# Optimization experiments

Measured on AMD Instinct MI355X. Metric: run time of the kernel, lower is better.

## Reference

```python
import jax, jax.numpy as jnp
import numpy as np


def _ring_mask(n, d, dtype):
    # concentric-square mask: ring index r = min(i, j, n-1-i, n-1-j);
    # outer d rings are 0, inner rings are 1; center forced to 1.
    i = jnp.arange(n)
    ri = jnp.minimum(i, n - 1 - i)  # [n]
    ring = jnp.minimum(ri[:, None], ri[None, :])  # [n, n]
    mask = (ring >= d).astype(dtype)
    w = (n + 1) // 2
    mask = mask.at[w - 1, w - 1].set(jnp.asarray(1, dtype))
    return mask


def _conv2d(x, w, b):
    # x: [B,1,2,C], w: [1,1,2,k] -> [B,1,1,C] (padding only along last axis)
    pad = (w.shape[3] - 1) // 2
    y = jax.lax.conv_general_dilated(
        x, w, window_strides=(1, 1), padding=((0, 0), (pad, pad)),
        dimension_numbers=('NCHW', 'OIHW', 'NCHW'))
    return y + b.reshape(1, 1, 1, 1)


def setup_inputs() -> dict:
    key = jax.random.key(0)
    k1, k2, k3, k4, k5 = jax.random.split(key, 5)
    B, C1, C2, P = 512, 16, 30, 15
    K = 5  # int((log2(480)+3)/2) made odd
    x = jax.random.normal(k1, (B, C1, C2, P, P), dtype=jnp.float32)
    w1 = jax.random.normal(k2, (1, 1, 2, K), dtype=jnp.float32) * 0.3
    b1 = jax.random.normal(k3, (1,), dtype=jnp.float32) * 0.1
    w2 = jax.random.normal(k4, (1, 1, 2, K), dtype=jnp.float32) * 0.3
    b2 = jax.random.normal(k5, (1,), dtype=jnp.float32) * 0.1
    return {"x": x, "w1": w1, "b1": b1, "w2": w2, "b2": b2}


def reference(x, w1, b1, w2, b2):
    B, C1, C2, H, W = x.shape
    C = C1 * C2
    out = x.reshape(B, C, H, W)
    d = (W - 1) // 2 - 1  # patch_size == W, ScaleMaskModule d
    mask = _ring_mask(W, d, x.dtype)  # [W, W]

    # masked branch: adaptive avg pool(1) == spatial mean of masked input
    out_x1 = (out * mask).mean(axis=(2, 3))  # [B, C]
    out_x2 = out_x1[:, ::-1]                 # reversed channel order
    out_xx = jnp.stack([out_x1, out_x2], axis=1)[:, None]  # [B,1,2,C]

    # plain branch
    out1 = out.mean(axis=(2, 3))  # [B, C]
    out2 = out1[:, ::-1]
    outx = jnp.stack([out1, out2], axis=1)[:, None]  # [B,1,2,C]

    a1 = jax.nn.sigmoid(_conv2d(outx, w1, b1))    # [B,1,1,C]
    a2 = jax.nn.sigmoid(_conv2d(out_xx, w2, b2))  # [B,1,1,C]
    at1 = jnp.transpose(a1 * a2, (0, 3, 1, 2))    # [B,C,1,1]
    at = jax.nn.sigmoid((at1 - 0.2) * 2)

    out = out * at
    return out.reshape(B, C1, C2, H, W)
```

## Files before the change

### kernel.cpp

```cpp
#include <hip/hip_runtime.h>
#include <math.h>

#define BB 512
#define CC 480
#define HW 225
#define CHW (CC * HW)
#define NF4 (CHW / 4)
#define NGRP (CC / 4)
#define NTHREADS 1024
#define NWAVES (NTHREADS / 64)

using f4 = __attribute__((ext_vector_type(4))) float;

__device__ __forceinline__ float sigmoidf(float v) {
    return 1.0f / (1.0f + __expf(-v));
}

__global__ __launch_bounds__(NTHREADS) void fused_kernel(
    const float* __restrict__ x,
    const float* __restrict__ w1, const float* __restrict__ b1,
    const float* __restrict__ w2, const float* __restrict__ b2,
    float* __restrict__ out)
{
    __shared__ float Ms[CC];
    __shared__ float Rs[CC];
    __shared__ float As[CC];

    const int b = blockIdx.x;
    const int t = threadIdx.x;
    const int wave = t >> 6;
    const int lane = t & 63;

    const f4* __restrict__ xb4 = (const f4*)(x + (long long)b * CHW);

    for (int gr = wave; gr < NGRP; gr += NWAVES) {
        const f4* gp = xb4 + gr * 225;
        float f0 = 0.f, f1 = 0.f, f2 = 0.f, f3 = 0.f;
        float r0 = 0.f, r1 = 0.f, r2 = 0.f, r3 = 0.f;
#pragma unroll
        for (int j = 0; j < 4; ++j) {
            const int idx = lane + 64 * j;
            if (idx < 225) {
                f4 v = gp[idx];
                const int e0 = 4 * idx;
#pragma unroll
                for (int jj = 0; jj < 4; ++jj) {
                    const int e = e0 + jj;
                    const float vv = v[jj];
                    const int q = (e >= 450) ? ((e >= 675) ? 3 : 2)
                                             : ((e >= 225) ? 1 : 0);
                    const int r = e - 225 * q;
                    const bool ring = (r >= 96 && r <= 98) ||
                                      (r >= 111 && r <= 113) ||
                                      (r >= 126 && r <= 128);
                    const float rv = ring ? vv : 0.f;
                    f0 += (q == 0) ? vv : 0.f;
                    f1 += (q == 1) ? vv : 0.f;
                    f2 += (q == 2) ? vv : 0.f;
                    f3 += (q == 3) ? vv : 0.f;
                    r0 += (q == 0) ? rv : 0.f;
                    r1 += (q == 1) ? rv : 0.f;
                    r2 += (q == 2) ? rv : 0.f;
                    r3 += (q == 3) ? rv : 0.f;
                }
            }
        }
#pragma unroll
        for (int off = 32; off > 0; off >>= 1) {
            f0 += __shfl_down(f0, off, 64);
            f1 += __shfl_down(f1, off, 64);
            f2 += __shfl_down(f2, off, 64);
            f3 += __shfl_down(f3, off, 64);
            r0 += __shfl_down(r0, off, 64);
            r1 += __shfl_down(r1, off, 64);
            r2 += __shfl_down(r2, off, 64);
            r3 += __shfl_down(r3, off, 64);
        }
        if (lane == 0) {
            const float s = 1.0f / 225.0f;
            Ms[4 * gr + 0] = f0 * s;  Rs[4 * gr + 0] = r0 * s;
            Ms[4 * gr + 1] = f1 * s;  Rs[4 * gr + 1] = r1 * s;
            Ms[4 * gr + 2] = f2 * s;  Rs[4 * gr + 2] = r2 * s;
            Ms[4 * gr + 3] = f3 * s;  Rs[4 * gr + 3] = r3 * s;
        }
    }
    __syncthreads();

    if (t < CC) {
        const int c = t;
        float g1 = b1[0], g2 = b2[0];
#pragma unroll
        for (int k = 0; k < 5; ++k) {
            const int j = c + k - 2;
            if (j >= 0 && j < CC) {
                g1 += w1[k] * Ms[j] + w1[5 + k] * Ms[CC - 1 - j];
                g2 += w2[k] * Rs[j] + w2[5 + k] * Rs[CC - 1 - j];
            }
        }
        As[c] = sigmoidf((sigmoidf(g1) * sigmoidf(g2) - 0.2f) * 2.0f);
    }
    __syncthreads();

    f4* __restrict__ ob4 = (f4*)(out + (long long)b * CHW);
    for (int g = t; g < NF4; g += NTHREADS) {
        f4 v = xb4[g];
        const int e0 = 4 * g;
        const int c0 = e0 / 225;
        const int rr = e0 - 225 * c0;
        const int c1 = c0 + (rr >= 224);
        const int c2 = c0 + (rr >= 223);
        const int c3 = c0 + (rr >= 222);
        v[0] *= As[c0];
        v[1] *= As[c1];
        v[2] *= As[c2];
        v[3] *= As[c3];
        __builtin_nontemporal_store(v, &ob4[g]);
    }
}

extern "C" void kernel_launch(void* const* d_in, const int* in_sizes, int n_in,
                              void* d_out, int out_size, void* d_ws, size_t ws_size,
                              hipStream_t stream)
{
    const float* x  = (const float*)d_in[0];
    const float* w1 = (const float*)d_in[1];
    const float* b1 = (const float*)d_in[2];
    const float* w2 = (const float*)d_in[3];
    const float* b2 = (const float*)d_in[4];
    float* out = (float*)d_out;

    fused_kernel<<<BB, NTHREADS, 0, stream>>>(x, w1, b1, w2, b2, out);
}
```

Baseline: 401.4 us.

## Split fused kernel into reduce, gate, and scale kernels for higher parallelism

Replaces the single per-batch fused kernel with three launches: a grid-stride reduction over all channel groups writing means to workspace, a small gate kernel computing the attention weights, and a chunked scale kernel using 8 blocks per batch. This is meant to raise occupancy and remove the in-block serialization between the reduction and scaling phases. It adds workspace traffic and two extra launches, and it drops any cache reuse of x between the two phases that a single block could have had.

After: 415.9 us. 3.6% more time.

```diff
diff --git a/kernel.cpp b/kernel.cpp
--- a/kernel.cpp
+++ b/kernel.cpp
@@ -7,8 +7,18 @@
 #define CHW (CC * HW)
 #define NF4 (CHW / 4)
 #define NGRP (CC / 4)
-#define NTHREADS 1024
-#define NWAVES (NTHREADS / 64)
+#define NGRP_TOTAL (BB * NGRP)
+
+#define RED_BLOCKS 1920
+#define RED_THREADS 256
+#define RED_WAVES (RED_BLOCKS * (RED_THREADS / 64))
+
+#define CHUNKS 8
+#define CHUNK_F4 (NF4 / CHUNKS)
+#define CHUNK_CH (CC / CHUNKS)
+#define SC_THREADS 256
+#define SC_FULL_ITERS (CHUNK_F4 / SC_THREADS)
+#define SC_TAIL (CHUNK_F4 - SC_FULL_ITERS * SC_THREADS)
 
 using f4 = __attribute__((ext_vector_type(4))) float;
 
@@ -16,25 +26,19 @@
     return 1.0f / (1.0f + __expf(-v));
 }
 
-__global__ __launch_bounds__(NTHREADS) void fused_kernel(
+__global__ __launch_bounds__(RED_THREADS) void reduce_kernel(
     const float* __restrict__ x,
-    const float* __restrict__ w1, const float* __restrict__ b1,
-    const float* __restrict__ w2, const float* __restrict__ b2,
-    float* __restrict__ out)
+    float* __restrict__ S, float* __restrict__ R)
 {
-    __shared__ float Ms[CC];
-    __shared__ float Rs[CC];
-    __shared__ float As[CC];
+    const int wave = threadIdx.x >> 6;
+    const int lane = threadIdx.x & 63;
+    const int gw0 = blockIdx.x * (RED_THREADS / 64) + wave;
 
-    const int b = blockIdx.x;
-    const int t = threadIdx.x;
-    const int wave = t >> 6;
-    const int lane = t & 63;
+    for (int gg = gw0; gg < NGRP_TOTAL; gg += RED_WAVES) {
+        const int b  = gg / NGRP;
+        const int gr = gg - b * NGRP;
+        const f4* __restrict__ gp = (const f4*)x + (long long)b * NF4 + gr * 225;
 
-    const f4* __restrict__ xb4 = (const f4*)(x + (long long)b * CHW);
-
-    for (int gr = wave; gr < NGRP; gr += NWAVES) {
-        const f4* gp = xb4 + gr * 225;
         float f0 = 0.f, f1 = 0.f, f2 = 0.f, f3 = 0.f;
         float r0 = 0.f, r1 = 0.f, r2 = 0.f, r3 = 0.f;
 #pragma unroll
@@ -78,16 +82,26 @@
         }
         if (lane == 0) {
             const float s = 1.0f / 225.0f;
-            Ms[4 * gr + 0] = f0 * s;  Rs[4 * gr + 0] = r0 * s;
-            Ms[4 * gr + 1] = f1 * s;  Rs[4 * gr + 1] = r1 * s;
-            Ms[4 * gr + 2] = f2 * s;  Rs[4 * gr + 2] = r2 * s;
-            Ms[4 * gr + 3] = f3 * s;  Rs[4 * gr + 3] = r3 * s;
+            const int base = b * CC + 4 * gr;
+            S[base + 0] = f0 * s;  R[base + 0] = r0 * s;
+            S[base + 1] = f1 * s;  R[base + 1] = r1 * s;
+            S[base + 2] = f2 * s;  R[base + 2] = r2 * s;
+            S[base + 3] = f3 * s;  R[base + 3] = r3 * s;
         }
     }
-    __syncthreads();
+}
 
-    if (t < CC) {
-        const int c = t;
+__global__ __launch_bounds__(512) void gate_kernel(
+    const float* __restrict__ S, const float* __restrict__ R,
+    const float* __restrict__ w1, const float* __restrict__ b1,
+    const float* __restrict__ w2, const float* __restrict__ b2,
+    float* __restrict__ G)
+{
+    const int b = blockIdx.x;
+    const int c = threadIdx.x;
+    if (c < CC) {
+        const float* __restrict__ Ms = S + b * CC;
+        const float* __restrict__ Rs = R + b * CC;
         float g1 = b1[0], g2 = b2[0];
 #pragma unroll
         for (int k = 0; k < 5; ++k) {
@@ -97,24 +111,50 @@
                 g2 += w2[k] * Rs[j] + w2[5 + k] * Rs[CC - 1 - j];
             }
         }
-        As[c] = sigmoidf((sigmoidf(g1) * sigmoidf(g2) - 0.2f) * 2.0f);
+        G[b * CC + c] = sigmoidf((sigmoidf(g1) * sigmoidf(g2) - 0.2f) * 2.0f);
     }
+}
+
+__global__ __launch_bounds__(SC_THREADS) void scale_kernel(
+    const float* __restrict__ x, const float* __restrict__ G,
+    float* __restrict__ out)
+{
+    __shared__ float As[CHUNK_CH];
+    const int blk = blockIdx.x;
+    const int b = blk >> 3;
+    const int s = blk & 7;
+    const int t = threadIdx.x;
+
+    if (t < CHUNK_CH) As[t] = G[b * CC + s * CHUNK_CH + t];
     __syncthreads();
 
-    f4* __restrict__ ob4 = (f4*)(out + (long long)b * CHW);
-    for (int g = t; g < NF4; g += NTHREADS) {
-        f4 v = xb4[g];
-        const int e0 = 4 * g;
-        const int c0 = e0 / 225;
-        const int rr = e0 - 225 * c0;
-        const int c1 = c0 + (rr >= 224);
-        const int c2 = c0 + (rr >= 223);
-        const int c3 = c0 + (rr >= 222);
-        v[0] *= As[c0];
-        v[1] *= As[c1];
-        v[2] *= As[c2];
-        v[3] *= As[c3];
-        __builtin_nontemporal_store(v, &ob4[g]);
+    const f4* __restrict__ xb = (const f4*)x + (long long)b * NF4 + s * CHUNK_F4;
+    f4* __restrict__ ob = (f4*)out + (long long)b * NF4 + s * CHUNK_F4;
+
+#pragma unroll 4
+    for (int k = 0; k < SC_FULL_ITERS; ++k) {
+        const int g = t + SC_THREADS * k;
+        f4 v = xb[g];
+        const int e = 4 * g;
+        const int c = e / 225;
+        const int rr = e - 225 * c;
+        v[0] *= As[c];
+        v[1] *= As[c + (rr >= 224)];
+        v[2] *= As[c + (rr >= 223)];
+        v[3] *= As[c + (rr >= 222)];
+        __builtin_nontemporal_store(v, &ob[g]);
+    }
+    if (t < SC_TAIL) {
+        const int g = SC_FULL_ITERS * SC_THREADS + t;
+        f4 v = xb[g];
+        const int e = 4 * g;
+        const int c = e / 225;
+        const int rr = e - 225 * c;
+        v[0] *= As[c];
+        v[1] *= As[c + (rr >= 224)];
+        v[2] *= As[c + (rr >= 223)];
+        v[3] *= As[c + (rr >= 222)];
+        __builtin_nontemporal_store(v, &ob[g]);
     }
 }
 
@@ -129,5 +169,11 @@
     const float* b2 = (const float*)d_in[4];
     float* out = (float*)d_out;
 
-    fused_kernel<<<BB, NTHREADS, 0, stream>>>(x, w1, b1, w2, b2, out);
+    float* S = (float*)d_ws;
+    float* R = S + BB * CC;
+    float* G = R + BB * CC;
+
+    reduce_kernel<<<RED_BLOCKS, RED_THREADS, 0, stream>>>(x, S, R);
+    gate_kernel<<<BB, 512, 0, stream>>>(S, R, w1, b1, w2, b2, G);
+    scale_kernel<<<BB * CHUNKS, SC_THREADS, 0, stream>>>(x, G, out);
 }
```
